# Kernel optimization log

Hardware: AMD Instinct MI355X
Metric: run time of the kernel (lower is better)

Reference implementation:

```python
import jax, jax.numpy as jnp
import numpy as np

N_FEAT = 1024
N_LAYER = 4  # n_layer + 1 in the original module


def setup_inputs() -> dict:
    key = jax.random.key(0)
    kx, kw, kb = jax.random.split(key, 3)
    x = jax.random.normal(kx, (16384, N_FEAT), dtype=jnp.float32)
    weight_w = jax.random.normal(kw, (N_LAYER, N_FEAT), dtype=jnp.float32)
    weight_b = jax.random.normal(kb, (N_LAYER, N_FEAT), dtype=jnp.float32)
    return {"x": x, "weight_w": weight_w, "weight_b": weight_b}


def reference(x, weight_w, weight_b):
    # Original per layer: x_{i+1} = x0 @ x_i^T @ w_i + b_i + x_i  (per sample).
    # (x0 x_i^T) w = x0 * <x_i, w>, so we use the O(n) equivalent form and
    # never materialize the [B, n, n] outer product.
    x0 = x  # [B, n]
    xi = x0
    for i in range(N_LAYER):
        xiw = jnp.einsum("bn,n->b", xi, weight_w[i])  # [B]
        xi = x0 * xiw[:, None] + weight_b[i][None, :] + xi
    return xi
```

## Files before the change

kernel.cpp:

```cpp
#include <hip/hip_runtime.h>

#define N_FEAT 1024
#define N_LAYER 4
#define R 8

__global__ __launch_bounds__(256) void crossnet_kernel(
    const float* __restrict__ x,
    const float* __restrict__ weight_w,
    const float* __restrict__ weight_b,
    float* __restrict__ out,
    int n_rows) {
  const int wave = threadIdx.x >> 6;
  const int lane = threadIdx.x & 63;
  const int row0 = (blockIdx.x * 4 + wave) * R;
  if (row0 >= n_rows) return;

  const float4* xq = (const float4*)x;
  float4* oq = (float4*)out;

  float4 x0[R * 4];
#pragma unroll
  for (int r = 0; r < R; ++r)
#pragma unroll
    for (int c = 0; c < 4; ++c)
      x0[r * 4 + c] = xq[(size_t)(row0 + r) * 256 + c * 64 + lane];

  float p[R * N_LAYER];
#pragma unroll
  for (int k = 0; k < R * N_LAYER; ++k) p[k] = 0.f;
  float e[N_LAYER] = {0.f, 0.f, 0.f, 0.f};
  float4 csum[4];

#pragma unroll
  for (int c = 0; c < 4; ++c) {
    float4 w[N_LAYER];
#pragma unroll
    for (int i = 0; i < N_LAYER; ++i)
      w[i] = ((const float4*)(weight_w + i * N_FEAT))[c * 64 + lane];

    float4 cum = make_float4(0.f, 0.f, 0.f, 0.f);
#pragma unroll
    for (int i = 0; i < N_LAYER; ++i) {
      if (i > 0)
        e[i] += cum.x * w[i].x + cum.y * w[i].y + cum.z * w[i].z + cum.w * w[i].w;
      float4 b = ((const float4*)(weight_b + i * N_FEAT))[c * 64 + lane];
      cum.x += b.x; cum.y += b.y; cum.z += b.z; cum.w += b.w;
    }
    csum[c] = cum;

#pragma unroll
    for (int r = 0; r < R; ++r) {
      const float4 xv = x0[r * 4 + c];
#pragma unroll
      for (int i = 0; i < N_LAYER; ++i) {
        p[r * N_LAYER + i] += xv.x * w[i].x + xv.y * w[i].y +
                              xv.z * w[i].z + xv.w * w[i].w;
      }
    }
  }

#pragma unroll
  for (int off = 32; off > 0; off >>= 1) {
#pragma unroll
    for (int k = 0; k < R * N_LAYER; ++k) p[k] += __shfl_xor(p[k], off, 64);
#pragma unroll
    for (int i = 1; i < N_LAYER; ++i) e[i] += __shfl_xor(e[i], off, 64);
  }

#pragma unroll
  for (int r = 0; r < R; ++r) {
    float A = 1.f;
#pragma unroll
    for (int i = 0; i < N_LAYER; ++i)
      A += A * p[r * N_LAYER + i] + e[i];

#pragma unroll
    for (int c = 0; c < 4; ++c) {
      const float4 xv = x0[r * 4 + c];
      float4 o;
      o.x = fmaf(xv.x, A, csum[c].x);
      o.y = fmaf(xv.y, A, csum[c].y);
      o.z = fmaf(xv.z, A, csum[c].z);
      o.w = fmaf(xv.w, A, csum[c].w);
      oq[(size_t)(row0 + r) * 256 + c * 64 + lane] = o;
    }
  }
}

extern "C" void kernel_launch(void* const* d_in, const int* in_sizes, int n_in,
                              void* d_out, int out_size, void* d_ws, size_t ws_size,
                              hipStream_t stream) {
  const float* x = (const float*)d_in[0];
  const float* ww = (const float*)d_in[1];
  const float* wb = (const float*)d_in[2];
  float* out = (float*)d_out;

  int n_rows = in_sizes[0] / N_FEAT;
  int rows_per_block = 4 * R;
  int n_blocks = (n_rows + rows_per_block - 1) / rows_per_block;
  crossnet_kernel<<<n_blocks, 256, 0, stream>>>(x, ww, wb, out, n_rows);
}
```

Measured before the change: 115.3 us.

## Split fused crossnet kernel into reduce and apply passes with grid-stride loops

Replaces the single fused kernel, which held eight rows of x per wave in registers, with two kernels. The first computes the four per-row dot products into a workspace buffer, and the second re-reads x to apply the scalar update using nontemporal stores. Both use grid-stride loops over rows with a fixed grid. This lowers register pressure and may raise occupancy, but x is now read twice from global memory (64 MB versus 32 MB for the input) and there is an extra launch.

```diff
diff --git a/kernel.cpp b/kernel.cpp
--- a/kernel.cpp
+++ b/kernel.cpp
@@ -2,87 +2,102 @@
 
 #define N_FEAT 1024
 #define N_LAYER 4
-#define R 8
 
-__global__ __launch_bounds__(256) void crossnet_kernel(
-    const float* __restrict__ x,
-    const float* __restrict__ weight_w,
-    const float* __restrict__ weight_b,
-    float* __restrict__ out,
-    int n_rows) {
+typedef float floatx4 __attribute__((ext_vector_type(4)));
+
+__device__ __forceinline__ float dot4(const float4 a, const float4 b) {
+  return fmaf(a.x, b.x, fmaf(a.y, b.y, fmaf(a.z, b.z, a.w * b.w)));
+}
+
+__global__ __launch_bounds__(256) void k_reduce(
+    const float* __restrict__ x, const float* __restrict__ weight_w,
+    float* __restrict__ p, int n_rows) {
   const int wave = threadIdx.x >> 6;
   const int lane = threadIdx.x & 63;
-  const int row0 = (blockIdx.x * 4 + wave) * R;
-  if (row0 >= n_rows) return;
+  const int gw = blockIdx.x * 4 + wave;
+  const int n_waves = gridDim.x * 4;
 
-  const float4* xq = (const float4*)x;
-  float4* oq = (float4*)out;
-
-  float4 x0[R * 4];
+  float4 w[N_LAYER][4];
 #pragma unroll
-  for (int r = 0; r < R; ++r)
+  for (int i = 0; i < N_LAYER; ++i)
 #pragma unroll
     for (int c = 0; c < 4; ++c)
-      x0[r * 4 + c] = xq[(size_t)(row0 + r) * 256 + c * 64 + lane];
+      w[i][c] = ((const float4*)(weight_w + i * N_FEAT))[c * 64 + lane];
 
-  float p[R * N_LAYER];
+  for (int row = gw; row < n_rows; row += n_waves) {
+    const float4* xr = (const float4*)(x + (size_t)row * N_FEAT);
+    float4 xv[4];
 #pragma unroll
-  for (int k = 0; k < R * N_LAYER; ++k) p[k] = 0.f;
+    for (int c = 0; c < 4; ++c) xv[c] = xr[c * 64 + lane];
+
+    float pp[N_LAYER] = {0.f, 0.f, 0.f, 0.f};
+#pragma unroll
+    for (int c = 0; c < 4; ++c)
+#pragma unroll
+      for (int i = 0; i < N_LAYER; ++i) pp[i] += dot4(xv[c], w[i][c]);
+
+#pragma unroll
+    for (int off = 32; off > 0; off >>= 1)
+#pragma unroll
+      for (int i = 0; i < N_LAYER; ++i) pp[i] += __shfl_xor(pp[i], off, 64);
+
+    if (lane == 0) {
+      float4 pv = make_float4(pp[0], pp[1], pp[2], pp[3]);
+      ((float4*)p)[row] = pv;
+    }
+  }
+}
+
+__global__ __launch_bounds__(256) void k_apply(
+    const float* __restrict__ x, const float* __restrict__ weight_w,
+    const float* __restrict__ weight_b, const float* __restrict__ p,
+    float* __restrict__ out, int n_rows) {
+  const int wave = threadIdx.x >> 6;
+  const int lane = threadIdx.x & 63;
+  const int gw = blockIdx.x * 4 + wave;
+  const int n_waves = gridDim.x * 4;
+
+  float4 csum[4];
   float e[N_LAYER] = {0.f, 0.f, 0.f, 0.f};
-  float4 csum[4];
-
 #pragma unroll
   for (int c = 0; c < 4; ++c) {
     float4 w[N_LAYER];
 #pragma unroll
     for (int i = 0; i < N_LAYER; ++i)
       w[i] = ((const float4*)(weight_w + i * N_FEAT))[c * 64 + lane];
-
     float4 cum = make_float4(0.f, 0.f, 0.f, 0.f);
 #pragma unroll
     for (int i = 0; i < N_LAYER; ++i) {
-      if (i > 0)
-        e[i] += cum.x * w[i].x + cum.y * w[i].y + cum.z * w[i].z + cum.w * w[i].w;
+      if (i > 0) e[i] += dot4(cum, w[i]);
       float4 b = ((const float4*)(weight_b + i * N_FEAT))[c * 64 + lane];
       cum.x += b.x; cum.y += b.y; cum.z += b.z; cum.w += b.w;
     }
     csum[c] = cum;
-
+  }
 #pragma unroll
-    for (int r = 0; r < R; ++r) {
-      const float4 xv = x0[r * 4 + c];
-#pragma unroll
-      for (int i = 0; i < N_LAYER; ++i) {
-        p[r * N_LAYER + i] += xv.x * w[i].x + xv.y * w[i].y +
-                              xv.z * w[i].z + xv.w * w[i].w;
-      }
-    }
-  }
-
-#pragma unroll
-  for (int off = 32; off > 0; off >>= 1) {
-#pragma unroll
-    for (int k = 0; k < R * N_LAYER; ++k) p[k] += __shfl_xor(p[k], off, 64);
+  for (int off = 32; off > 0; off >>= 1)
 #pragma unroll
     for (int i = 1; i < N_LAYER; ++i) e[i] += __shfl_xor(e[i], off, 64);
-  }
 
-#pragma unroll
-  for (int r = 0; r < R; ++r) {
+  for (int row = gw; row < n_rows; row += n_waves) {
+    const float4 pv = ((const float4*)p)[row];
     float A = 1.f;
-#pragma unroll
-    for (int i = 0; i < N_LAYER; ++i)
-      A += A * p[r * N_LAYER + i] + e[i];
+    A = fmaf(A, pv.x, A);
+    A = fmaf(A, pv.y, A + e[1]);
+    A = fmaf(A, pv.z, A + e[2]);
+    A = fmaf(A, pv.w, A + e[3]);
 
+    const float4* xr = (const float4*)(x + (size_t)row * N_FEAT);
+    floatx4* orow = (floatx4*)(out + (size_t)row * N_FEAT);
 #pragma unroll
     for (int c = 0; c < 4; ++c) {
-      const float4 xv = x0[r * 4 + c];
-      float4 o;
+      float4 xv = xr[c * 64 + lane];
+      floatx4 o;
       o.x = fmaf(xv.x, A, csum[c].x);
       o.y = fmaf(xv.y, A, csum[c].y);
       o.z = fmaf(xv.z, A, csum[c].z);
       o.w = fmaf(xv.w, A, csum[c].w);
-      oq[(size_t)(row0 + r) * 256 + c * 64 + lane] = o;
+      __builtin_nontemporal_store(o, &orow[c * 64 + lane]);
     }
   }
 }
@@ -94,9 +109,9 @@
   const float* ww = (const float*)d_in[1];
   const float* wb = (const float*)d_in[2];
   float* out = (float*)d_out;
+  float* p = (float*)d_ws;
 
   int n_rows = in_sizes[0] / N_FEAT;
-  int rows_per_block = 4 * R;
-  int n_blocks = (n_rows + rows_per_block - 1) / rows_per_block;
-  crossnet_kernel<<<n_blocks, 256, 0, stream>>>(x, ww, wb, out, n_rows);
+  k_reduce<<<2048, 256, 0, stream>>>(x, ww, p, n_rows);
+  k_apply<<<2048, 256, 0, stream>>>(x, ww, wb, p, out, n_rows);
 }
```

New measurement: 125.0 us. +8.4%, slower.
